# Performance work log

Measured on AMD Instinct MI355X. Metric: run time of the kernel, lower is better.

Reference implementation:

```python
import jax, jax.numpy as jnp
import numpy as np

N_NODES = 50000
N_EDGES = 800000
NFEAT, NHID, NCLASS = 512, 128, 40
PN_SCALE = 1.0


def spmm(edge_row, edge_col, edge_val, h):
    # sparse [N,N] @ dense [N,F]: out[r] += val * h[c] for each edge (r, c)
    msgs = edge_val[:, None] * h[edge_col]  # [E, F]
    return jax.ops.segment_sum(msgs, edge_row, num_segments=N_NODES)


def pair_norm(x):
    # mode 'PN': center columns, scale by mean row norm
    x = x - x.mean(axis=0)
    rownorm_mean = jnp.sqrt(1e-6 + (x * x).sum(axis=1).mean())
    return PN_SCALE * x / rownorm_mean


def setup_inputs() -> dict:
    key = jax.random.key(0)
    ks = jax.random.split(key, 12)

    def uinit(k, shape, fan_out):
        stdv = 1.0 / np.sqrt(fan_out)
        return jax.random.uniform(k, shape, jnp.float32, -stdv, stdv)

    return {
        "x": jax.random.normal(ks[0], (N_NODES, NFEAT), jnp.float32),
        "edge_row": jax.random.randint(ks[1], (N_EDGES,), 0, N_NODES),
        "edge_col": jax.random.randint(ks[2], (N_EDGES,), 0, N_NODES),
        "edge_val": jax.random.uniform(ks[3], (N_EDGES,), jnp.float32),
        "W0": uinit(ks[4], (NFEAT, NHID), NHID),
        "b0": uinit(ks[5], (1, NHID), NHID),
        "W1": uinit(ks[6], (NHID, NHID), NHID),
        "b1": uinit(ks[7], (1, NHID), NHID),
        "W2": uinit(ks[8], (NHID, NHID), NHID),
        "b2": uinit(ks[9], (1, NHID), NHID),
        "W_out": uinit(ks[10], (NHID, NCLASS), NCLASS),
        "b_out": uinit(ks[11], (1, NCLASS), NCLASS),
    }


def reference(x, edge_row, edge_col, edge_val,
              W0, b0, W1, b1, W2, b2, W_out, b_out):
    # DeepGCN forward, eval mode (dropout p=0 is identity), residual=1 -> skip every layer
    x_old = 0.0
    for W, b in ((W0, b0), (W1, b1), (W2, b2)):
        h = x @ W                             # dense mm
        h = spmm(edge_row, edge_col, edge_val, h) + b  # sparse aggregate + bias
        h = pair_norm(h)
        h = jax.nn.relu(h)
        h = h + x_old                         # residual (x_old=0 on first layer)
        x_old = h
        x = h
    out = spmm(edge_row, edge_col, edge_val, x @ W_out) + b_out
    return out
```

## Files before the change

kernel.cpp:

```cpp
#include <hip/hip_runtime.h>
#include <hip/hip_bf16.h>
#include <math.h>

#define N_NODES 50000
#define N_EDGES 800000
#define NFEAT   512
#define NHID    128
#define NCLASS  40
#define NPASS    4
#define ROWS_PER_PASS (N_NODES / NPASS)
#define NCB      8
#define CB_W     (N_NODES / NCB)
#define NCNT     (N_NODES * NCB)
#define SCAN_BLOCKS ((NCNT + 1023) / 1024)
#define NSTAT    132
#define NB_STATS 256

typedef short bf16x8 __attribute__((ext_vector_type(8)));
typedef float f32x4  __attribute__((ext_vector_type(4)));

__device__ inline float bf2f(unsigned short u) {
    union { unsigned int i; float f; } x; x.i = ((unsigned int)u) << 16; return x.f;
}

__global__ void hist_kernel(const int* __restrict__ rows, const int* __restrict__ cols,
                            int* __restrict__ cnt, int n) {
    int i = blockIdx.x * blockDim.x + threadIdx.x;
    if (i < n) {
        int r = rows[i];
        int cb = cols[i] / CB_W;
        atomicAdd(&cnt[r * NCB + cb], 1);
    }
}

__global__ __launch_bounds__(1024) void scan_p1_kernel(const int* __restrict__ cnt,
                                                       int* __restrict__ bsum, int n) {
    int i = blockIdx.x * 1024 + threadIdx.x;
    int v = (i < n) ? cnt[i] : 0;
    __shared__ int sm[16];
    int lane = threadIdx.x & 63, w = threadIdx.x >> 6;
    #pragma unroll
    for (int off = 32; off > 0; off >>= 1) v += __shfl_xor(v, off, 64);
    if (lane == 0) sm[w] = v;
    __syncthreads();
    if (threadIdx.x == 0) {
        int s = 0;
        #pragma unroll
        for (int j = 0; j < 16; ++j) s += sm[j];
        bsum[blockIdx.x] = s;
    }
}

__global__ __launch_bounds__(512) void scan_p2_kernel(int* __restrict__ bsum, int nb) {
    __shared__ int wsum[8];
    int t = threadIdx.x;
    int lane = t & 63, w = t >> 6;
    int v = (t < nb) ? bsum[t] : 0;
    int x = v;
    #pragma unroll
    for (int off = 1; off < 64; off <<= 1) {
        int y = __shfl_up(x, off, 64);
        if (lane >= off) x += y;
    }
    if (lane == 63) wsum[w] = x;
    __syncthreads();
    int wbase = 0;
    for (int j = 0; j < w; ++j) wbase += wsum[j];
    if (t < nb) bsum[t] = wbase + x - v;
}

__global__ __launch_bounds__(1024) void scan_p3_kernel(const int* __restrict__ cnt,
                                                       const int* __restrict__ bsum,
                                                       int* __restrict__ bptr,
                                                       int* __restrict__ cursor, int n) {
    __shared__ int wsum[16];
    int b = blockIdx.x;
    int i = b * 1024 + threadIdx.x;
    int lane = threadIdx.x & 63, w = threadIdx.x >> 6;
    int v = (i < n) ? cnt[i] : 0;
    int x = v;
    #pragma unroll
    for (int off = 1; off < 64; off <<= 1) {
        int y = __shfl_up(x, off, 64);
        if (lane >= off) x += y;
    }
    if (lane == 63) wsum[w] = x;
    __syncthreads();
    int wbase = 0;
    for (int j = 0; j < w; ++j) wbase += wsum[j];
    int incl = bsum[b] + wbase + x;
    if (i < n) {
        bptr[i + 1] = incl;
        cursor[i] = incl - v;
    }
    if (i == 0) bptr[0] = 0;
}

__global__ void scatter_kernel(const int* __restrict__ rows, const int* __restrict__ cols,
                               const float* __restrict__ vals, int* __restrict__ cursor,
                               int2* __restrict__ csr_cv, int n, int blocksPerPass) {
    int p = blockIdx.x / blocksPerPass;
    int b = blockIdx.x % blocksPerPass;
    int i = b * 256 + threadIdx.x;
    if (i >= n) return;
    int r = rows[i];
    int lo = p * ROWS_PER_PASS;
    if (r < lo || r >= lo + ROWS_PER_PASS) return;
    int c = cols[i];
    int pos = atomicAdd(&cursor[r * NCB + c / CB_W], 1);
    csr_cv[pos] = make_int2(c, __float_as_int(vals[i]));
}

__global__ __launch_bounds__(256) void wt_cvt_all_kernel(const float* __restrict__ W0,
        const float* __restrict__ W1, const float* __restrict__ W2,
        const float* __restrict__ Wo, __hip_bfloat16* __restrict__ Wt0,
        __hip_bfloat16* __restrict__ Wt1, __hip_bfloat16* __restrict__ Wt2,
        __hip_bfloat16* __restrict__ Wot) {
    int i = blockIdx.x * blockDim.x + threadIdx.x;
    if (i < 65536) {
        int k = i >> 7, n = i & 127;
        Wt0[(size_t)n * 512 + k] = __float2bfloat16(W0[i]);
    } else if (i < 65536 + 16384) {
        int j = i - 65536; int k = j >> 7, n = j & 127;
        Wt1[(size_t)n * 128 + k] = __float2bfloat16(W1[j]);
    } else if (i < 65536 + 32768) {
        int j = i - 65536 - 16384; int k = j >> 7, n = j & 127;
        Wt2[(size_t)n * 128 + k] = __float2bfloat16(W2[j]);
    } else if (i < 65536 + 32768 + 8192) {
        int j = i - 65536 - 32768; int k = j >> 6, n = j & 63;
        float v = (n < NCLASS) ? Wo[k * NCLASS + n] : 0.f;
        Wot[(size_t)n * 128 + k] = __float2bfloat16(v);
    }
}

template<int BM, int BN, int K>
__global__ __launch_bounds__(256) void mfma_gemm_f32a(const float* __restrict__ Xg,
                                                      const __hip_bfloat16* __restrict__ Wt,
                                                      __hip_bfloat16* __restrict__ Ob,
                                                      float* __restrict__ stats_out, int M) {
    constexpr int BK  = 64;
    constexpr int LDK = 72;
    constexpr int WN  = BN / 64;
    __shared__ short As[BM * LDK];
    __shared__ short Bs[BN * LDK];
    int t = threadIdx.x;
    if (blockIdx.x == 0 && t < NSTAT) stats_out[t] = 0.f;
    int lane = t & 63;
    int w = t >> 6;
    int wm = w / WN, wn = w % WN;
    int row0 = blockIdx.x * BM;
    int m0 = wm * 32, n0 = wn * 64;
    int l15 = lane & 15, quad = lane >> 4;

    f32x4 acc[2][4] = {};

    for (int k0 = 0; k0 < K; k0 += BK) {
        #pragma unroll
        for (int idx = t; idx < BM * 16; idx += 256) {
            int r = idx >> 4, c = idx & 15;
            float4 v = make_float4(0.f, 0.f, 0.f, 0.f);
            if (row0 + r < M)
                v = *(const float4*)(Xg + (size_t)(row0 + r) * K + k0 + c * 4);
            __hip_bfloat16 o[4] = {__float2bfloat16(v.x), __float2bfloat16(v.y),
                                   __float2bfloat16(v.z), __float2bfloat16(v.w)};
            *(short4*)(As + r * LDK + c * 4) = *(short4*)o;
        }
        #pragma unroll
        for (int idx = t; idx < BN * 8; idx += 256) {
            int r = idx >> 3, c = idx & 7;
            uint4 v = *(const uint4*)(Wt + (size_t)r * K + k0 + c * 8);
            *(uint4*)(Bs + r * LDK + c * 8) = v;
        }
        __syncthreads();
        #pragma unroll
        for (int ks = 0; ks < 2; ++ks) {
            bf16x8 af[2], bfv[4];
            #pragma unroll
            for (int mt = 0; mt < 2; ++mt)
                af[mt] = *(const bf16x8*)(As + (m0 + mt * 16 + l15) * LDK + ks * 32 + quad * 8);
            #pragma unroll
            for (int nt = 0; nt < 4; ++nt)
                bfv[nt] = *(const bf16x8*)(Bs + (n0 + nt * 16 + l15) * LDK + ks * 32 + quad * 8);
            #pragma unroll
            for (int mt = 0; mt < 2; ++mt)
                #pragma unroll
                for (int nt = 0; nt < 4; ++nt)
                    acc[mt][nt] = __builtin_amdgcn_mfma_f32_16x16x32_bf16(
                        af[mt], bfv[nt], acc[mt][nt], 0, 0, 0);
        }
        __syncthreads();
    }
    #pragma unroll
    for (int mt = 0; mt < 2; ++mt) {
        #pragma unroll
        for (int reg = 0; reg < 4; ++reg) {
            int row = row0 + m0 + mt * 16 + quad * 4 + reg;
            if (row < M) {
                #pragma unroll
                for (int nt = 0; nt < 4; ++nt)
                    Ob[(size_t)row * BN + n0 + nt * 16 + l15] =
                        __float2bfloat16(acc[mt][nt][reg]);
            }
        }
    }
}

template<int BM, int BN, bool ADD_RESID, bool WRITE_X>
__global__ __launch_bounds__(256) void mfma_gemm_pn(const __hip_bfloat16* __restrict__ Bm,
                                                    __hip_bfloat16* __restrict__ Xb,
                                                    const float* __restrict__ stats_in,
                                                    float* __restrict__ stats_out,
                                                    const __hip_bfloat16* __restrict__ Wt,
                                                    __hip_bfloat16* __restrict__ Ob, int M) {
    constexpr int K = 128, BK = 64, LDK = 72;
    constexpr int WN = BN / 64;
    __shared__ short As[BM * LDK];
    __shared__ short Bs[BN * LDK];
    __shared__ float smu[128];
    __shared__ float sred[128];
    __shared__ float sscale;
    int t = threadIdx.x;
    if (stats_out && blockIdx.x == 0 && t < NSTAT) stats_out[t] = 0.f;
    if (t < 128) {
        float mu = stats_in[t] * (1.0f / N_NODES);
        smu[t] = mu;
        sred[t] = mu * mu;
    }
    __syncthreads();
    for (int off = 64; off > 0; off >>= 1) {
        if (t < off) sred[t] += sred[t + off];
        __syncthreads();
    }
    if (t == 0) {
        float ms = stats_in[128] * (1.0f / N_NODES) - sred[0];
        sscale = 1.0f / sqrtf(1e-6f + ms);
    }
    __syncthreads();
    float sc = sscale;

    int lane = t & 63;
    int w = t >> 6;
    int wm = w / WN, wn = w % WN;
    int row0 = blockIdx.x * BM;
    int m0 = wm * 32, n0 = wn * 64;
    int l15 = lane & 15, quad = lane >> 4;

    f32x4 acc[2][4] = {};

    for (int k0 = 0; k0 < K; k0 += BK) {
        #pragma unroll
        for (int idx = t; idx < BM * 8; idx += 256) {
            int r = idx >> 3, c = idx & 7;
            int gr = row0 + r;
            int k = k0 + c * 8;
            uint4 bm = make_uint4(0u, 0u, 0u, 0u);
            uint4 xo = make_uint4(0u, 0u, 0u, 0u);
            bool ok = gr < M;
            if (ok) bm = *(const uint4*)(Bm + (size_t)gr * 128 + k);
            if (ADD_RESID && ok) xo = *(const uint4*)(Xb + (size_t)gr * 128 + k);
            unsigned short* bu = (unsigned short*)&bm;
            unsigned short* xu = (unsigned short*)&xo;
            __hip_bfloat16 o[8];
            #pragma unroll
            for (int j = 0; j < 8; ++j) {
                float v = fmaxf((bf2f(bu[j]) - smu[k + j]) * sc, 0.f);
                if (ADD_RESID) v += bf2f(xu[j]);
                o[j] = __float2bfloat16(v);
            }
            *(uint4*)(As + r * LDK + c * 8) = *(uint4*)o;
            if (WRITE_X && ok) *(uint4*)(Xb + (size_t)gr * 128 + k) = *(uint4*)o;
        }
        #pragma unroll
        for (int idx = t; idx < BN * 8; idx += 256) {
            int r = idx >> 3, c = idx & 7;
            uint4 v = *(const uint4*)(Wt + (size_t)r * K + k0 + c * 8);
            *(uint4*)(Bs + r * LDK + c * 8) = v;
        }
        __syncthreads();
        #pragma unroll
        for (int ks = 0; ks < 2; ++ks) {
            bf16x8 af[2], bfv[4];
            #pragma unroll
            for (int mt = 0; mt < 2; ++mt)
                af[mt] = *(const bf16x8*)(As + (m0 + mt * 16 + l15) * LDK + ks * 32 + quad * 8);
            #pragma unroll
            for (int nt = 0; nt < 4; ++nt)
                bfv[nt] = *(const bf16x8*)(Bs + (n0 + nt * 16 + l15) * LDK + ks * 32 + quad * 8);
            #pragma unroll
            for (int mt = 0; mt < 2; ++mt)
                #pragma unroll
                for (int nt = 0; nt < 4; ++nt)
                    acc[mt][nt] = __builtin_amdgcn_mfma_f32_16x16x32_bf16(
                        af[mt], bfv[nt], acc[mt][nt], 0, 0, 0);
        }
        __syncthreads();
    }
    #pragma unroll
    for (int mt = 0; mt < 2; ++mt) {
        #pragma unroll
        for (int reg = 0; reg < 4; ++reg) {
            int row = row0 + m0 + mt * 16 + quad * 4 + reg;
            if (row < M) {
                #pragma unroll
                for (int nt = 0; nt < 4; ++nt)
                    Ob[(size_t)row * BN + n0 + nt * 16 + l15] =
                        __float2bfloat16(acc[mt][nt][reg]);
            }
        }
    }
}

__global__ __launch_bounds__(256) void spmm_bf16_kernel(const __hip_bfloat16* __restrict__ H,
                                                        const int* __restrict__ bptr,
                                                        const int2* __restrict__ cv,
                                                        const float* __restrict__ bias,
                                                        __hip_bfloat16* __restrict__ Bm,
                                                        int nrows) {
    int wid = (int)((blockIdx.x * blockDim.x + threadIdx.x) >> 6);
    wid = __builtin_amdgcn_readfirstlane(wid);
    int lane = threadIdx.x & 63;
    int h = lane >> 5;
    int sub = lane & 31;
    if (wid >= nrows) return;
    int s = bptr[wid * NCB];
    int e = bptr[wid * NCB + NCB];
    const ushort4* H4 = (const ushort4*)H;
    f32x4 acc = {0.f, 0.f, 0.f, 0.f};
    int i = s;
    for (; i + 7 < e; i += 8) {
        int2 c0 = cv[i],     c1 = cv[i + 1], c2 = cv[i + 2], c3 = cv[i + 3];
        int2 c4 = cv[i + 4], c5 = cv[i + 5], c6 = cv[i + 6], c7 = cv[i + 7];
        int   ka = h ? c4.x : c0.x;  float va = __int_as_float(h ? c4.y : c0.y);
        int   kb = h ? c5.x : c1.x;  float vb = __int_as_float(h ? c5.y : c1.y);
        int   kc = h ? c6.x : c2.x;  float vc = __int_as_float(h ? c6.y : c2.y);
        int   kd = h ? c7.x : c3.x;  float vd = __int_as_float(h ? c7.y : c3.y);
        ushort4 ga = H4[(size_t)ka * 32 + sub];
        ushort4 gb = H4[(size_t)kb * 32 + sub];
        ushort4 gc = H4[(size_t)kc * 32 + sub];
        ushort4 gd = H4[(size_t)kd * 32 + sub];
        acc[0] = fmaf(va, bf2f(ga.x), acc[0]); acc[1] = fmaf(va, bf2f(ga.y), acc[1]);
        acc[2] = fmaf(va, bf2f(ga.z), acc[2]); acc[3] = fmaf(va, bf2f(ga.w), acc[3]);
        acc[0] = fmaf(vb, bf2f(gb.x), acc[0]); acc[1] = fmaf(vb, bf2f(gb.y), acc[1]);
        acc[2] = fmaf(vb, bf2f(gb.z), acc[2]); acc[3] = fmaf(vb, bf2f(gb.w), acc[3]);
        acc[0] = fmaf(vc, bf2f(gc.x), acc[0]); acc[1] = fmaf(vc, bf2f(gc.y), acc[1]);
        acc[2] = fmaf(vc, bf2f(gc.z), acc[2]); acc[3] = fmaf(vc, bf2f(gc.w), acc[3]);
        acc[0] = fmaf(vd, bf2f(gd.x), acc[0]); acc[1] = fmaf(vd, bf2f(gd.y), acc[1]);
        acc[2] = fmaf(vd, bf2f(gd.z), acc[2]); acc[3] = fmaf(vd, bf2f(gd.w), acc[3]);
    }
    for (; i + 3 < e; i += 4) {
        int2 c0 = cv[i], c1 = cv[i + 1], c2 = cv[i + 2], c3 = cv[i + 3];
        int   ka = h ? c2.x : c0.x;  float va = __int_as_float(h ? c2.y : c0.y);
        int   kb = h ? c3.x : c1.x;  float vb = __int_as_float(h ? c3.y : c1.y);
        ushort4 ga = H4[(size_t)ka * 32 + sub];
        ushort4 gb = H4[(size_t)kb * 32 + sub];
        acc[0] = fmaf(va, bf2f(ga.x), acc[0]); acc[1] = fmaf(va, bf2f(ga.y), acc[1]);
        acc[2] = fmaf(va, bf2f(ga.z), acc[2]); acc[3] = fmaf(va, bf2f(ga.w), acc[3]);
        acc[0] = fmaf(vb, bf2f(gb.x), acc[0]); acc[1] = fmaf(vb, bf2f(gb.y), acc[1]);
        acc[2] = fmaf(vb, bf2f(gb.z), acc[2]); acc[3] = fmaf(vb, bf2f(gb.w), acc[3]);
    }
    for (; i < e; ++i) {
        int2 c = cv[i];
        if (h == 0) {
            float v = __int_as_float(c.y);
            ushort4 g = H4[(size_t)c.x * 32 + sub];
            acc[0] = fmaf(v, bf2f(g.x), acc[0]); acc[1] = fmaf(v, bf2f(g.y), acc[1]);
            acc[2] = fmaf(v, bf2f(g.z), acc[2]); acc[3] = fmaf(v, bf2f(g.w), acc[3]);
        }
    }
    #pragma unroll
    for (int c = 0; c < 4; ++c) acc[c] += __shfl_xor(acc[c], 32);
    if (h == 0) {
        float4 b4 = *(const float4*)(bias + 4 * sub);
        __hip_bfloat16 o[4] = {__float2bfloat16(acc[0] + b4.x), __float2bfloat16(acc[1] + b4.y),
                               __float2bfloat16(acc[2] + b4.z), __float2bfloat16(acc[3] + b4.w)};
        *(ushort4*)(Bm + (size_t)wid * 128 + 4 * sub) = *(ushort4*)o;
    }
}

__global__ __launch_bounds__(256) void stats_kernel(const __hip_bfloat16* __restrict__ B,
                                                    float* __restrict__ stats, int n2) {
    int tid = blockIdx.x * blockDim.x + threadIdx.x;
    int stride = NB_STATS * 256;
    const __hip_bfloat162* B2 = (const __hip_bfloat162*)B;
    float cs0 = 0.f, cs1 = 0.f, sq = 0.f;
    for (int j = tid; j < n2; j += stride) {
        __hip_bfloat162 h = B2[j];
        float a = __bfloat162float(h.x), b = __bfloat162float(h.y);
        cs0 += a; cs1 += b;
        sq = fmaf(a, a, sq); sq = fmaf(b, b, sq);
    }
    __shared__ float s0[256], s1[256], ss[256];
    int t = threadIdx.x;
    s0[t] = cs0; s1[t] = cs1; ss[t] = sq;
    __syncthreads();
    if (t < 64) {
        float a = s0[t] + s0[t + 64] + s0[t + 128] + s0[t + 192];
        float b = s1[t] + s1[t + 64] + s1[t + 128] + s1[t + 192];
        atomicAdd(&stats[2 * t], a);
        atomicAdd(&stats[2 * t + 1], b);
    }
    __syncthreads();
    for (int off = 128; off > 0; off >>= 1) {
        if (t < off) ss[t] += ss[t + off];
        __syncthreads();
    }
    if (t == 0) atomicAdd(&stats[128], ss[0]);
}

__global__ __launch_bounds__(256) void spmm_out_kernel(const __hip_bfloat16* __restrict__ G,
                                                       const int* __restrict__ bptr,
                                                       const int2* __restrict__ cv,
                                                       const float* __restrict__ bias,
                                                       float* __restrict__ out, int nrows) {
    int wid = (int)((blockIdx.x * blockDim.x + threadIdx.x) >> 6);
    wid = __builtin_amdgcn_readfirstlane(wid);
    int lane = threadIdx.x & 63;
    int h = lane >> 5;
    int sub = lane & 31;
    if (wid >= nrows) return;
    int s = bptr[wid * NCB];
    int e = bptr[wid * NCB + NCB];
    const __hip_bfloat162* G2 = (const __hip_bfloat162*)G;
    float a0 = 0.f, a1 = 0.f;
    int i = s;
    for (; i + 7 < e; i += 8) {
        int2 c0 = cv[i],     c1 = cv[i + 1], c2 = cv[i + 2], c3 = cv[i + 3];
        int2 c4 = cv[i + 4], c5 = cv[i + 5], c6 = cv[i + 6], c7 = cv[i + 7];
        int   ka = h ? c4.x : c0.x;  float va = __int_as_float(h ? c4.y : c0.y);
        int   kb = h ? c5.x : c1.x;  float vb = __int_as_float(h ? c5.y : c1.y);
        int   kc = h ? c6.x : c2.x;  float vc = __int_as_float(h ? c6.y : c2.y);
        int   kd = h ? c7.x : c3.x;  float vd = __int_as_float(h ? c7.y : c3.y);
        __hip_bfloat162 ga = G2[(size_t)ka * 32 + sub];
        __hip_bfloat162 gb = G2[(size_t)kb * 32 + sub];
        __hip_bfloat162 gc = G2[(size_t)kc * 32 + sub];
        __hip_bfloat162 gd = G2[(size_t)kd * 32 + sub];
        a0 = fmaf(va, __bfloat162float(ga.x), a0); a1 = fmaf(va, __bfloat162float(ga.y), a1);
        a0 = fmaf(vb, __bfloat162float(gb.x), a0); a1 = fmaf(vb, __bfloat162float(gb.y), a1);
        a0 = fmaf(vc, __bfloat162float(gc.x), a0); a1 = fmaf(vc, __bfloat162float(gc.y), a1);
        a0 = fmaf(vd, __bfloat162float(gd.x), a0); a1 = fmaf(vd, __bfloat162float(gd.y), a1);
    }
    for (; i + 3 < e; i += 4) {
        int2 c0 = cv[i], c1 = cv[i + 1], c2 = cv[i + 2], c3 = cv[i + 3];
        int   ka = h ? c2.x : c0.x;  float va = __int_as_float(h ? c2.y : c0.y);
        int   kb = h ? c3.x : c1.x;  float vb = __int_as_float(h ? c3.y : c1.y);
        __hip_bfloat162 ga = G2[(size_t)ka * 32 + sub];
        __hip_bfloat162 gb = G2[(size_t)kb * 32 + sub];
        a0 = fmaf(va, __bfloat162float(ga.x), a0); a1 = fmaf(va, __bfloat162float(ga.y), a1);
        a0 = fmaf(vb, __bfloat162float(gb.x), a0); a1 = fmaf(vb, __bfloat162float(gb.y), a1);
    }
    for (; i < e; ++i) {
        int2 c = cv[i];
        if (h == 0) {
            float v = __int_as_float(c.y);
            __hip_bfloat162 g = G2[(size_t)c.x * 32 + sub];
            a0 = fmaf(v, __bfloat162float(g.x), a0);
            a1 = fmaf(v, __bfloat162float(g.y), a1);
        }
    }
    a0 += __shfl_xor(a0, 32);
    a1 += __shfl_xor(a1, 32);
    if (h == 0 && sub < NCLASS / 2) {
        float2 b2 = *(const float2*)(bias + 2 * sub);
        float2 o = make_float2(a0 + b2.x, a1 + b2.y);
        *(float2*)(out + (size_t)wid * NCLASS + 2 * sub) = o;
    }
}

extern "C" void kernel_launch(void* const* d_in, const int* in_sizes, int n_in,
                              void* d_out, int out_size, void* d_ws, size_t ws_size,
                              hipStream_t stream) {
    const float* x        = (const float*)d_in[0];
    const int*   edge_row = (const int*)  d_in[1];
    const int*   edge_col = (const int*)  d_in[2];
    const float* edge_val = (const float*)d_in[3];
    const float* W0 = (const float*)d_in[4];
    const float* b0 = (const float*)d_in[5];
    const float* W1 = (const float*)d_in[6];
    const float* b1 = (const float*)d_in[7];
    const float* W2 = (const float*)d_in[8];
    const float* b2 = (const float*)d_in[9];
    const float* W_out = (const float*)d_in[10];
    const float* b_out = (const float*)d_in[11];
    float* out = (float*)d_out;

    const size_t NH = (size_t)N_NODES * NHID;

    char* p = (char*)d_ws;
    __hip_bfloat16* Xb   = (__hip_bfloat16*)p;  p += NH * 2;
    __hip_bfloat16* A_bf = (__hip_bfloat16*)p;  p += NH * 2;
    __hip_bfloat16* Bm   = (__hip_bfloat16*)p;  p += NH * 2;
    __hip_bfloat16* Wt0 = (__hip_bfloat16*)p;   p += (size_t)128 * 512 * 2;
    __hip_bfloat16* Wt1 = (__hip_bfloat16*)p;   p += (size_t)128 * 128 * 2;
    __hip_bfloat16* Wt2 = (__hip_bfloat16*)p;   p += (size_t)128 * 128 * 2;
    __hip_bfloat16* Wot = (__hip_bfloat16*)p;   p += (size_t)64 * 128 * 2;
    float* statsA   = (float*)p;                p += NSTAT * 4;
    float* statsB   = (float*)p;                p += NSTAT * 4;
    int* cnt      = (int*)p;                    p += (size_t)NCNT * 4;
    int* bptr     = (int*)p;                    p += (size_t)(NCNT + 1) * 4 + 4;
    int* cursor   = (int*)p;                    p += (size_t)NCNT * 4;
    int* bsum     = (int*)p;                    p += (size_t)SCAN_BLOCKS * 4 + 4;
    int2* csr_cv  = (int2*)p;                   p += (size_t)N_EDGES * 8;

    const int EB = (N_EDGES + 255) / 256;
    const int SPMM_GRID = (N_NODES + 3) / 4;

    wt_cvt_all_kernel<<<(65536 + 32768 + 8192 + 255) / 256, 256, 0, stream>>>(
        W0, W1, W2, W_out, Wt0, Wt1, Wt2, Wot);

    hipMemsetAsync(cnt, 0, NCNT * sizeof(int), stream);
    hist_kernel<<<EB, 256, 0, stream>>>(edge_row, edge_col, cnt, N_EDGES);
    scan_p1_kernel<<<SCAN_BLOCKS, 1024, 0, stream>>>(cnt, bsum, NCNT);
    scan_p2_kernel<<<1, 512, 0, stream>>>(bsum, SCAN_BLOCKS);
    scan_p3_kernel<<<SCAN_BLOCKS, 1024, 0, stream>>>(cnt, bsum, bptr, cursor, NCNT);
    scatter_kernel<<<EB * NPASS, 256, 0, stream>>>(edge_row, edge_col, edge_val, cursor,
                                                   csr_cv, N_EDGES, EB);

    mfma_gemm_f32a<64, 128, 512><<<(N_NODES + 63) / 64, 256, 0, stream>>>(
        x, Wt0, A_bf, statsA, N_NODES);
    spmm_bf16_kernel<<<SPMM_GRID, 256, 0, stream>>>(A_bf, bptr, csr_cv, b0, Bm, N_NODES);
    stats_kernel<<<NB_STATS, 256, 0, stream>>>(Bm, statsA, (int)(NH / 2));

    mfma_gemm_pn<64, 128, false, true><<<(N_NODES + 63) / 64, 256, 0, stream>>>(
        Bm, Xb, statsA, statsB, Wt1, A_bf, N_NODES);
    spmm_bf16_kernel<<<SPMM_GRID, 256, 0, stream>>>(A_bf, bptr, csr_cv, b1, Bm, N_NODES);
    stats_kernel<<<NB_STATS, 256, 0, stream>>>(Bm, statsB, (int)(NH / 2));

    mfma_gemm_pn<64, 128, true, true><<<(N_NODES + 63) / 64, 256, 0, stream>>>(
        Bm, Xb, statsB, statsA, Wt2, A_bf, N_NODES);
    spmm_bf16_kernel<<<SPMM_GRID, 256, 0, stream>>>(A_bf, bptr, csr_cv, b2, Bm, N_NODES);
    stats_kernel<<<NB_STATS, 256, 0, stream>>>(Bm, statsA, (int)(NH / 2));

    mfma_gemm_pn<128, 64, true, false><<<(N_NODES + 127) / 128, 256, 0, stream>>>(
        Bm, Xb, statsA, nullptr, Wot, A_bf, N_NODES);
    spmm_out_kernel<<<(N_NODES + 3) / 4, 256, 0, stream>>>(A_bf, bptr, csr_cv, b_out,
                                                           out, N_NODES);
}
```

Baseline: 495.9 us.

## Double column-bucket count and deepen SpMM gather unrolling to sixteen edges

Raises the number of column buckets per row from 8 to 16 so that edges within each CSR row are sorted more finely by column, which should improve locality of the gathered feature rows. The scan second pass is widened to 1024 threads because the block count now exceeds 512. The SpMM kernels gain a 16-edge main loop in which each half-wave loads eight contiguous edges and issues eight gathers before accumulating, and the smaller loops index per half directly instead of selecting with branches. The trade-offs are a histogram and scan that are twice as large, plus higher register pressure in the SpMM kernels.

```diff
diff --git a/kernel.cpp b/kernel.cpp
--- a/kernel.cpp
+++ b/kernel.cpp
@@ -9,7 +9,7 @@
 #define NCLASS  40
 #define NPASS    4
 #define ROWS_PER_PASS (N_NODES / NPASS)
-#define NCB      8
+#define NCB      16
 #define CB_W     (N_NODES / NCB)
 #define NCNT     (N_NODES * NCB)
 #define SCAN_BLOCKS ((NCNT + 1023) / 1024)
@@ -51,8 +51,8 @@
     }
 }
 
-__global__ __launch_bounds__(512) void scan_p2_kernel(int* __restrict__ bsum, int nb) {
-    __shared__ int wsum[8];
+__global__ __launch_bounds__(1024) void scan_p2_kernel(int* __restrict__ bsum, int nb) {
+    __shared__ int wsum[16];
     int t = threadIdx.x;
     int lane = t & 63, w = t >> 6;
     int v = (t < nb) ? bsum[t] : 0;
@@ -327,32 +327,39 @@
     const ushort4* H4 = (const ushort4*)H;
     f32x4 acc = {0.f, 0.f, 0.f, 0.f};
     int i = s;
+    for (; i + 15 < e; i += 16) {
+        int2 cc[8];
+        #pragma unroll
+        for (int j = 0; j < 8; ++j) cc[j] = cv[i + 8 * h + j];
+        ushort4 g[8];
+        #pragma unroll
+        for (int j = 0; j < 8; ++j) g[j] = H4[(size_t)cc[j].x * 32 + sub];
+        #pragma unroll
+        for (int j = 0; j < 8; ++j) {
+            float v = __int_as_float(cc[j].y);
+            acc[0] = fmaf(v, bf2f(g[j].x), acc[0]); acc[1] = fmaf(v, bf2f(g[j].y), acc[1]);
+            acc[2] = fmaf(v, bf2f(g[j].z), acc[2]); acc[3] = fmaf(v, bf2f(g[j].w), acc[3]);
+        }
+    }
     for (; i + 7 < e; i += 8) {
-        int2 c0 = cv[i],     c1 = cv[i + 1], c2 = cv[i + 2], c3 = cv[i + 3];
-        int2 c4 = cv[i + 4], c5 = cv[i + 5], c6 = cv[i + 6], c7 = cv[i + 7];
-        int   ka = h ? c4.x : c0.x;  float va = __int_as_float(h ? c4.y : c0.y);
-        int   kb = h ? c5.x : c1.x;  float vb = __int_as_float(h ? c5.y : c1.y);
-        int   kc = h ? c6.x : c2.x;  float vc = __int_as_float(h ? c6.y : c2.y);
-        int   kd = h ? c7.x : c3.x;  float vd = __int_as_float(h ? c7.y : c3.y);
-        ushort4 ga = H4[(size_t)ka * 32 + sub];
-        ushort4 gb = H4[(size_t)kb * 32 + sub];
-        ushort4 gc = H4[(size_t)kc * 32 + sub];
-        ushort4 gd = H4[(size_t)kd * 32 + sub];
-        acc[0] = fmaf(va, bf2f(ga.x), acc[0]); acc[1] = fmaf(va, bf2f(ga.y), acc[1]);
-        acc[2] = fmaf(va, bf2f(ga.z), acc[2]); acc[3] = fmaf(va, bf2f(ga.w), acc[3]);
-        acc[0] = fmaf(vb, bf2f(gb.x), acc[0]); acc[1] = fmaf(vb, bf2f(gb.y), acc[1]);
-        acc[2] = fmaf(vb, bf2f(gb.z), acc[2]); acc[3] = fmaf(vb, bf2f(gb.w), acc[3]);
-        acc[0] = fmaf(vc, bf2f(gc.x), acc[0]); acc[1] = fmaf(vc, bf2f(gc.y), acc[1]);
-        acc[2] = fmaf(vc, bf2f(gc.z), acc[2]); acc[3] = fmaf(vc, bf2f(gc.w), acc[3]);
-        acc[0] = fmaf(vd, bf2f(gd.x), acc[0]); acc[1] = fmaf(vd, bf2f(gd.y), acc[1]);
-        acc[2] = fmaf(vd, bf2f(gd.z), acc[2]); acc[3] = fmaf(vd, bf2f(gd.w), acc[3]);
+        int2 cc[4];
+        #pragma unroll
+        for (int j = 0; j < 4; ++j) cc[j] = cv[i + 4 * h + j];
+        ushort4 g[4];
+        #pragma unroll
+        for (int j = 0; j < 4; ++j) g[j] = H4[(size_t)cc[j].x * 32 + sub];
+        #pragma unroll
+        for (int j = 0; j < 4; ++j) {
+            float v = __int_as_float(cc[j].y);
+            acc[0] = fmaf(v, bf2f(g[j].x), acc[0]); acc[1] = fmaf(v, bf2f(g[j].y), acc[1]);
+            acc[2] = fmaf(v, bf2f(g[j].z), acc[2]); acc[3] = fmaf(v, bf2f(g[j].w), acc[3]);
+        }
     }
     for (; i + 3 < e; i += 4) {
-        int2 c0 = cv[i], c1 = cv[i + 1], c2 = cv[i + 2], c3 = cv[i + 3];
-        int   ka = h ? c2.x : c0.x;  float va = __int_as_float(h ? c2.y : c0.y);
-        int   kb = h ? c3.x : c1.x;  float vb = __int_as_float(h ? c3.y : c1.y);
-        ushort4 ga = H4[(size_t)ka * 32 + sub];
-        ushort4 gb = H4[(size_t)kb * 32 + sub];
+        int2 c0 = cv[i + 2 * h], c1 = cv[i + 2 * h + 1];
+        ushort4 ga = H4[(size_t)c0.x * 32 + sub];
+        ushort4 gb = H4[(size_t)c1.x * 32 + sub];
+        float va = __int_as_float(c0.y), vb = __int_as_float(c1.y);
         acc[0] = fmaf(va, bf2f(ga.x), acc[0]); acc[1] = fmaf(va, bf2f(ga.y), acc[1]);
         acc[2] = fmaf(va, bf2f(ga.z), acc[2]); acc[3] = fmaf(va, bf2f(ga.w), acc[3]);
         acc[0] = fmaf(vb, bf2f(gb.x), acc[0]); acc[1] = fmaf(vb, bf2f(gb.y), acc[1]);
@@ -423,28 +430,39 @@
     const __hip_bfloat162* G2 = (const __hip_bfloat162*)G;
     float a0 = 0.f, a1 = 0.f;
     int i = s;
+    for (; i + 15 < e; i += 16) {
+        int2 cc[8];
+        #pragma unroll
+        for (int j = 0; j < 8; ++j) cc[j] = cv[i + 8 * h + j];
+        __hip_bfloat162 g[8];
+        #pragma unroll
+        for (int j = 0; j < 8; ++j) g[j] = G2[(size_t)cc[j].x * 32 + sub];
+        #pragma unroll
+        for (int j = 0; j < 8; ++j) {
+            float v = __int_as_float(cc[j].y);
+            a0 = fmaf(v, __bfloat162float(g[j].x), a0);
+            a1 = fmaf(v, __bfloat162float(g[j].y), a1);
+        }
+    }
     for (; i + 7 < e; i += 8) {
-        int2 c0 = cv[i],     c1 = cv[i + 1], c2 = cv[i + 2], c3 = cv[i + 3];
-        int2 c4 = cv[i + 4], c5 = cv[i + 5], c6 = cv[i + 6], c7 = cv[i + 7];
-        int   ka = h ? c4.x : c0.x;  float va = __int_as_float(h ? c4.y : c0.y);
-        int   kb = h ? c5.x : c1.x;  float vb = __int_as_float(h ? c5.y : c1.y);
-        int   kc = h ? c6.x : c2.x;  float vc = __int_as_float(h ? c6.y : c2.y);
-        int   kd = h ? c7.x : c3.x;  float vd = __int_as_float(h ? c7.y : c3.y);
-        __hip_bfloat162 ga = G2[(size_t)ka * 32 + sub];
-        __hip_bfloat162 gb = G2[(size_t)kb * 32 + sub];
-        __hip_bfloat162 gc = G2[(size_t)kc * 32 + sub];
-        __hip_bfloat162 gd = G2[(size_t)kd * 32 + sub];
-        a0 = fmaf(va, __bfloat162float(ga.x), a0); a1 = fmaf(va, __bfloat162float(ga.y), a1);
-        a0 = fmaf(vb, __bfloat162float(gb.x), a0); a1 = fmaf(vb, __bfloat162float(gb.y), a1);
-        a0 = fmaf(vc, __bfloat162float(gc.x), a0); a1 = fmaf(vc, __bfloat162float(gc.y), a1);
-        a0 = fmaf(vd, __bfloat162float(gd.x), a0); a1 = fmaf(vd, __bfloat162float(gd.y), a1);
+        int2 cc[4];
+        #pragma unroll
+        for (int j = 0; j < 4; ++j) cc[j] = cv[i + 4 * h + j];
+        __hip_bfloat162 g[4];
+        #pragma unroll
+        for (int j = 0; j < 4; ++j) g[j] = G2[(size_t)cc[j].x * 32 + sub];
+        #pragma unroll
+        for (int j = 0; j < 4; ++j) {
+            float v = __int_as_float(cc[j].y);
+            a0 = fmaf(v, __bfloat162float(g[j].x), a0);
+            a1 = fmaf(v, __bfloat162float(g[j].y), a1);
+        }
     }
     for (; i + 3 < e; i += 4) {
-        int2 c0 = cv[i], c1 = cv[i + 1], c2 = cv[i + 2], c3 = cv[i + 3];
-        int   ka = h ? c2.x : c0.x;  float va = __int_as_float(h ? c2.y : c0.y);
-        int   kb = h ? c3.x : c1.x;  float vb = __int_as_float(h ? c3.y : c1.y);
-        __hip_bfloat162 ga = G2[(size_t)ka * 32 + sub];
-        __hip_bfloat162 gb = G2[(size_t)kb * 32 + sub];
+        int2 c0 = cv[i + 2 * h], c1 = cv[i + 2 * h + 1];
+        __hip_bfloat162 ga = G2[(size_t)c0.x * 32 + sub];
+        __hip_bfloat162 gb = G2[(size_t)c1.x * 32 + sub];
+        float va = __int_as_float(c0.y), vb = __int_as_float(c1.y);
         a0 = fmaf(va, __bfloat162float(ga.x), a0); a1 = fmaf(va, __bfloat162float(ga.y), a1);
         a0 = fmaf(vb, __bfloat162float(gb.x), a0); a1 = fmaf(vb, __bfloat162float(gb.y), a1);
     }
@@ -510,7 +528,7 @@
     hipMemsetAsync(cnt, 0, NCNT * sizeof(int), stream);
     hist_kernel<<<EB, 256, 0, stream>>>(edge_row, edge_col, cnt, N_EDGES);
     scan_p1_kernel<<<SCAN_BLOCKS, 1024, 0, stream>>>(cnt, bsum, NCNT);
-    scan_p2_kernel<<<1, 512, 0, stream>>>(bsum, SCAN_BLOCKS);
+    scan_p2_kernel<<<1, 1024, 0, stream>>>(bsum, SCAN_BLOCKS);
     scan_p3_kernel<<<SCAN_BLOCKS, 1024, 0, stream>>>(cnt, bsum, bptr, cursor, NCNT);
     scatter_kernel<<<EB * NPASS, 256, 0, stream>>>(edge_row, edge_col, edge_val, cursor,
                                                    csr_cv, N_EDGES, EB);
```

New measurement: 502.0 us. No clear change (+1.2%).
